# Optimization experiments

Hardware: AMD Instinct MI355X
Metric: run time of the kernel (lower is better)

The kernel has to match this reference:

```python
import jax, jax.numpy as jnp
import numpy as np

WORD_DEPTH, K, K2, L, FL, J = 128, 128, 128, 64, 3, 2


def conv1d(x, w, b):
    # x: [B, C, T], w: [O, I, k], VALID padding (matches nn.Conv1d default)
    y = jax.lax.conv_general_dilated(x, w, (1,), 'VALID',
                                     dimension_numbers=('NCH', 'OIH', 'NCH'))
    return y + b[None, :, None]


def encode(x, w1, b1, w2, b2, ws, bs):
    # x: [B, T, D] -> semantic vector [B, L]
    h = jnp.tanh(conv1d(x.transpose(0, 2, 1), w1, b1))   # [B, K, T-2]
    h = jnp.tanh(conv1d(h, w2, b2))                      # [B, K2, T-4]
    h = h.max(axis=2)                                    # kmax pooling, k=1
    return jnp.tanh(h @ ws.T + bs)                       # [B, L]


def setup_inputs() -> dict:
    key = jax.random.key(0)
    ks = jax.random.split(key, 20)
    B, T = 64, 2048
    s = 0.05
    return {
        'q':    jax.random.normal(ks[0], (B, T, WORD_DEPTH), jnp.float32),
        'pos':  jax.random.normal(ks[1], (B, T, WORD_DEPTH), jnp.float32),
        'negs': jax.random.normal(ks[2], (J, B, T, WORD_DEPTH), jnp.float32),
        'qw1': jax.random.normal(ks[3], (K, WORD_DEPTH, FL), jnp.float32) * s,
        'qb1': jnp.zeros((K,), jnp.float32),
        'qw2': jax.random.normal(ks[4], (K2, K, FL), jnp.float32) * s,
        'qb2': jnp.zeros((K2,), jnp.float32),
        'qsw': jax.random.normal(ks[5], (L, K2), jnp.float32) * s,
        'qsb': jnp.zeros((L,), jnp.float32),
        'dw1': jax.random.normal(ks[6], (K, WORD_DEPTH, FL), jnp.float32) * s,
        'db1': jnp.zeros((K,), jnp.float32),
        'dw2': jax.random.normal(ks[7], (K2, K, FL), jnp.float32) * s,
        'db2': jnp.zeros((K2,), jnp.float32),
        'dsw': jax.random.normal(ks[8], (L, K2), jnp.float32) * s,
        'dsb': jnp.zeros((L,), jnp.float32),
        'gw':  jnp.asarray(1.0, jnp.float32),   # learn_gamma Conv1d(1,1,1) weight
        'gb':  jnp.asarray(0.0, jnp.float32),   # learn_gamma bias
    }


def reference(q, pos, negs, qw1, qb1, qw2, qb2, qsw, qsb,
              dw1, db1, dw2, db2, dsw, dsb, gw, gb):
    Jn, B, T, D = negs.shape
    q_s = encode(q, qw1, qb1, qw2, qb2, qsw, qsb)                  # [B, L]
    pos_s = encode(pos, dw1, db1, dw2, db2, dsw, dsb)              # [B, L]
    neg_s = encode(negs.reshape(Jn * B, T, D),
                   dw1, db1, dw2, db2, dsw, dsb).reshape(Jn, B, L)
    pos_dot = jnp.einsum('bl,bl->b', q_s, pos_s)                   # [B]
    neg_dot = jnp.einsum('bl,jbl->bj', q_s, neg_s)                 # [B, J]
    dots = jnp.concatenate([pos_dot[:, None], neg_dot], axis=1)   # [B, J+1]
    with_gamma = gw * dots + gb                                    # conv1x1
    return jax.nn.softmax(with_gamma, axis=1)                      # [B, J+1]
```

## Files before the change

### kernel.cpp

```cpp
#include <hip/hip_runtime.h>
#include <stdint.h>


typedef __bf16 bf16x8 __attribute__((ext_vector_type(8)));
typedef __bf16 bf16x4 __attribute__((ext_vector_type(4)));
typedef float f32x16 __attribute__((ext_vector_type(16)));
typedef unsigned short u16x8 __attribute__((ext_vector_type(8)));

__device__ __forceinline__ unsigned short f2bf(float f) {
  unsigned u = __builtin_bit_cast(unsigned, f);
  u = u + 0x7FFFu + ((u >> 16) & 1u);
  return (unsigned short)(u >> 16);
}

__device__ __forceinline__ float fast_tanh(float x) {
  x = fminf(10.0f, fmaxf(-10.0f, x));
  float t = __builtin_amdgcn_exp2f(x * -2.8853900817779268f);
  return (1.0f - t) * __builtin_amdgcn_rcpf(1.0f + t);
}

__global__ void prep_kernel(const float* __restrict__ qw1, const float* __restrict__ qw2,
                            const float* __restrict__ dw1, const float* __restrict__ dw2,
                            unsigned short* __restrict__ W1f, unsigned short* __restrict__ W2f) {
  int gid = blockIdx.x * 256 + threadIdx.x;
  int which = gid >= 98304;
  int e = which ? gid - 98304 : gid;
  int br = e / 49152; int r = e % 49152;
  int f = r / 16384; int r2 = r & 16383;
  int kk = r2 >> 11; int row = (r2 >> 4) & 127; int hi = (r2 >> 3) & 1; int j = r2 & 7;
  int c = kk * 16 + hi * 8 + j;
  const float* src = which ? (br ? dw2 : qw2) : (br ? dw1 : qw1);
  (which ? W2f : W1f)[e] = f2bf(src[row * 384 + c * 3 + f]);
}

#define XS0    0
#define XBUF   16384
#define H1S0   32768
#define HBUF   15872
#define B1_OFF 64512
#define LDS_TOTAL 65024
#define YS 60
#define NWIN 35
#define TOUT 2044

__global__ __launch_bounds__(512) void cdssm_main(
    const float* __restrict__ q, const float* __restrict__ pos, const float* __restrict__ negs,
    const unsigned short* __restrict__ W1f, const unsigned short* __restrict__ W2f,
    const float* __restrict__ qb1, const float* __restrict__ db1,
    float* __restrict__ hpart) {
  extern __shared__ char lds[];
  const int tid = threadIdx.x;
  const int seq = blockIdx.x;
  const int branch = (seq < 64) ? 0 : 1;
  const float* xptr = (seq < 64) ? (q + (size_t)seq * 2048 * 128)
                    : (seq < 128) ? (pos + (size_t)(seq - 64) * 2048 * 128)
                                  : (negs + (size_t)(seq - 128) * 2048 * 128);
  const float* b1g = branch ? db1 : qb1;

  if (tid < 128) ((float*)(lds + B1_OFF))[tid] = b1g[tid];

  const int lane = tid & 63;
  const int w = tid >> 6;
  const int lrow = lane & 31;
  const int hi5 = lane >> 5;
  const int role = w >> 2;
  const int kt = w & 3;
  const int hi16 = hi5 * 16;

  const unsigned short* wfb = (role ? W2f : W1f) + (size_t)branch * 49152
                              + (kt * 32 + lrow) * 16 + hi5 * 8;

  bf16x8 ap[16];
#pragma unroll
  for (int f = 0; f < 2; ++f)
#pragma unroll
    for (int kk = 0; kk < 8; ++kk)
      ap[f * 8 + kk] = __builtin_bit_cast(bf16x8,
          *(const u16x8*)(wfb + f * 16384 + kk * 2048));

  float vmax[16];
#pragma unroll
  for (int r = 0; r < 16; ++r) vmax[r] = -1e30f;

  const int slot_s = tid >> 4;
  const int d0_s = (tid & 15) * 8;

#pragma unroll
  for (int u = 0; u < 2; ++u) {
    int sl = slot_s + u * 32;
    int t = sl;
    const float* src = xptr + ((size_t)t * 128 + d0_s);
    float4 v0 = *(const float4*)src;
    float4 v1 = *(const float4*)(src + 4);
    bf16x8 o;
    o[0] = (__bf16)v0.x; o[1] = (__bf16)v0.y; o[2] = (__bf16)v0.z; o[3] = (__bf16)v0.w;
    o[4] = (__bf16)v1.x; o[5] = (__bf16)v1.y; o[6] = (__bf16)v1.z; o[7] = (__bf16)v1.w;
    *(bf16x8*)(lds + XS0 + sl * 256 + ((d0_s * 2) ^ ((sl & 15) << 4))) = o;
  }
  __syncthreads();

  for (int i = 0; i <= NWIN; ++i) {
    float4 va[4];
    const bool doStage = (i < NWIN - 1);
    if (doStage) {
      const int tb = (i + 1) * YS;
#pragma unroll
      for (int u = 0; u < 2; ++u) {
        int t = tb + slot_s + u * 32; if (t > 2047) t = 2047;
        const float* src = xptr + ((size_t)t * 128 + d0_s);
        va[2 * u]     = *(const float4*)src;
        va[2 * u + 1] = *(const float4*)(src + 4);
      }
    }

    if (role == 0) {
      if (i < NWIN) {
        const int xb = XS0 + (i & 1) * XBUF;
        f32x16 acc0, acc1;
#pragma unroll
        for (int r = 0; r < 16; ++r) { acc0[r] = 0.f; acc1[r] = 0.f; }
        __builtin_amdgcn_s_setprio(1);
#pragma unroll
        for (int f = 0; f < 2; ++f) {
          int sv0 = lrow + f;
          int sv1 = 32 + lrow + f; if (sv1 > 63) sv1 = 63;
          int b0 = xb + sv0 * 256, z0 = (sv0 & 15) << 4;
          int b1 = xb + sv1 * 256, z1 = (sv1 & 15) << 4;
#pragma unroll
          for (int kk = 0; kk < 8; ++kk) {
            int ko = kk * 32 + hi16;
            bf16x8 bv0 = __builtin_bit_cast(bf16x8,
                *(const u16x8*)(lds + b0 + (ko ^ z0)));
            acc0 = __builtin_amdgcn_mfma_f32_32x32x16_bf16(ap[f * 8 + kk], bv0, acc0, 0, 0, 0);
            bf16x8 bv1 = __builtin_bit_cast(bf16x8,
                *(const u16x8*)(lds + b1 + (ko ^ z1)));
            acc1 = __builtin_amdgcn_mfma_f32_32x32x16_bf16(ap[f * 8 + kk], bv1, acc1, 0, 0, 0);
          }
        }
        {
          int sv0 = lrow + 2;
          int sv1 = 32 + lrow + 2; if (sv1 > 63) sv1 = 63;
          int b0 = xb + sv0 * 256, z0 = (sv0 & 15) << 4;
          int b1 = xb + sv1 * 256, z1 = (sv1 & 15) << 4;
#pragma unroll
          for (int kk = 0; kk < 8; ++kk) {
            bf16x8 av = __builtin_bit_cast(bf16x8,
                *(const u16x8*)(wfb + 2 * 16384 + kk * 2048));
            int ko = kk * 32 + hi16;
            bf16x8 bv0 = __builtin_bit_cast(bf16x8,
                *(const u16x8*)(lds + b0 + (ko ^ z0)));
            acc0 = __builtin_amdgcn_mfma_f32_32x32x16_bf16(av, bv0, acc0, 0, 0, 0);
            bf16x8 bv1 = __builtin_bit_cast(bf16x8,
                *(const u16x8*)(lds + b1 + (ko ^ z1)));
            acc1 = __builtin_amdgcn_mfma_f32_32x32x16_bf16(av, bv1, acc1, 0, 0, 0);
          }
        }
        __builtin_amdgcn_s_setprio(0);
        const int hb = H1S0 + (i & 1) * HBUF;
#pragma unroll
        for (int p = 0; p < 2; ++p) {
          const f32x16 acc = p ? acc1 : acc0;
          int s = p * 32 + lrow;
          if (s < 62) {
            int wb2 = hb + s * 256;
            int wz = (s & 15) << 4;
#pragma unroll
            for (int qd = 0; qd < 4; ++qd) {
              int k0 = kt * 32 + qd * 8 + hi5 * 4;
              float4 bq = *(const float4*)(lds + B1_OFF + k0 * 4);
              bf16x4 hv;
              hv[0] = (__bf16)fast_tanh(acc[qd * 4 + 0] + bq.x);
              hv[1] = (__bf16)fast_tanh(acc[qd * 4 + 1] + bq.y);
              hv[2] = (__bf16)fast_tanh(acc[qd * 4 + 2] + bq.z);
              hv[3] = (__bf16)fast_tanh(acc[qd * 4 + 3] + bq.w);
              *(bf16x4*)(lds + wb2 + ((k0 * 2) ^ wz)) = hv;
            }
          }
        }
      }
    } else {
      if (i >= 1) {
        const int hb = H1S0 + ((i & 1) ^ 1) * HBUF;
        f32x16 acc0, acc1;
#pragma unroll
        for (int r = 0; r < 16; ++r) { acc0[r] = 0.f; acc1[r] = 0.f; }
        __builtin_amdgcn_s_setprio(1);
#pragma unroll
        for (int f = 0; f < 2; ++f) {
          int sv0 = lrow + f;
          int sv1 = 32 + lrow + f; if (sv1 > 61) sv1 = 61;
          int b0 = hb + sv0 * 256, z0 = (sv0 & 15) << 4;
          int b1 = hb + sv1 * 256, z1 = (sv1 & 15) << 4;
#pragma unroll
          for (int kk = 0; kk < 8; ++kk) {
            int ko = kk * 32 + hi16;
            bf16x8 bv0 = __builtin_bit_cast(bf16x8,
                *(const u16x8*)(lds + b0 + (ko ^ z0)));
            acc0 = __builtin_amdgcn_mfma_f32_32x32x16_bf16(ap[f * 8 + kk], bv0, acc0, 0, 0, 0);
            bf16x8 bv1 = __builtin_bit_cast(bf16x8,
                *(const u16x8*)(lds + b1 + (ko ^ z1)));
            acc1 = __builtin_amdgcn_mfma_f32_32x32x16_bf16(ap[f * 8 + kk], bv1, acc1, 0, 0, 0);
          }
        }
        {
          int sv0 = lrow + 2;
          int sv1 = 32 + lrow + 2; if (sv1 > 61) sv1 = 61;
          int b0 = hb + sv0 * 256, z0 = (sv0 & 15) << 4;
          int b1 = hb + sv1 * 256, z1 = (sv1 & 15) << 4;
#pragma unroll
          for (int kk = 0; kk < 8; ++kk) {
            bf16x8 av = __builtin_bit_cast(bf16x8,
                *(const u16x8*)(wfb + 2 * 16384 + kk * 2048));
            int ko = kk * 32 + hi16;
            bf16x8 bv0 = __builtin_bit_cast(bf16x8,
                *(const u16x8*)(lds + b0 + (ko ^ z0)));
            acc0 = __builtin_amdgcn_mfma_f32_32x32x16_bf16(av, bv0, acc0, 0, 0, 0);
            bf16x8 bv1 = __builtin_bit_cast(bf16x8,
                *(const u16x8*)(lds + b1 + (ko ^ z1)));
            acc1 = __builtin_amdgcn_mfma_f32_32x32x16_bf16(av, bv1, acc1, 0, 0, 0);
          }
        }
        __builtin_amdgcn_s_setprio(0);
        const int base = (i - 1) * YS;
        const bool valid0 = (base + lrow < TOUT);
        const int s2b = 32 + lrow;
        const bool valid1 = (s2b < YS) && (base + s2b < TOUT);
#pragma unroll
        for (int r = 0; r < 16; ++r) {
          float v0 = valid0 ? acc0[r] : -1e30f;
          float v1 = valid1 ? acc1[r] : -1e30f;
          vmax[r] = fmaxf(vmax[r], fmaxf(v0, v1));
        }
      }
    }

    if (doStage) {
      const int xbn = XS0 + ((i + 1) & 1) * XBUF;
#pragma unroll
      for (int u = 0; u < 2; ++u) {
        int sl = slot_s + u * 32;
        const float* f0 = (const float*)&va[2 * u];
        bf16x8 o;
#pragma unroll
        for (int j = 0; j < 8; ++j) o[j] = (__bf16)f0[j];
        *(bf16x8*)(lds + xbn + sl * 256 + ((d0_s * 2) ^ ((sl & 15) << 4))) = o;
      }
    }
    __syncthreads();
  }

  if (role == 1) {
#pragma unroll
    for (int r = 0; r < 16; ++r) {
      float v = vmax[r];
      v = fmaxf(v, __shfl_xor(v, 1, 64));
      v = fmaxf(v, __shfl_xor(v, 2, 64));
      v = fmaxf(v, __shfl_xor(v, 4, 64));
      v = fmaxf(v, __shfl_xor(v, 8, 64));
      v = fmaxf(v, __shfl_xor(v, 16, 64));
      vmax[r] = v;
    }
  }
  float* hbuf = (float*)(lds + XS0);
  if (role == 1 && lrow == 0) {
#pragma unroll
    for (int r = 0; r < 16; ++r) {
      int rl = (r & 3) + 8 * (r >> 2) + 4 * hi5;
      hbuf[kt * 32 + rl] = vmax[r];
    }
  }
  __syncthreads();
  if (tid < 128) hpart[(size_t)seq * 128 + tid] = hbuf[tid];
}

__global__ void k2_proj(const float* __restrict__ hpart,
                        const float* __restrict__ qsw, const float* __restrict__ qsb,
                        const float* __restrict__ dsw, const float* __restrict__ dsb,
                        const float* __restrict__ qb2, const float* __restrict__ db2,
                        float* __restrict__ s_out) {
  int seq = blockIdx.x;
  int l = threadIdx.x;
  const float* sw = (seq < 64) ? qsw : dsw;
  const float* sb = (seq < 64) ? qsb : dsb;
  const float* b2 = (seq < 64) ? qb2 : db2;
  const float* h0 = hpart + (size_t)seq * 128;
  float acc = sb[l];
  for (int k = 0; k < 128; ++k)
    acc += fast_tanh(h0[k] + b2[k]) * sw[l * 128 + k];
  s_out[(size_t)seq * 64 + l] = fast_tanh(acc);
}

__global__ void k3_softmax(const float* __restrict__ s_out,
                           const float* __restrict__ gw, const float* __restrict__ gb,
                           float* __restrict__ out) {
  int b = threadIdx.x;
  const float* qs = s_out + (size_t)b * 64;
  const float* ps = s_out + (size_t)(64 + b) * 64;
  const float* n0 = s_out + (size_t)(128 + b) * 64;
  const float* n1 = s_out + (size_t)(192 + b) * 64;
  float d0 = 0.f, d1 = 0.f, d2 = 0.f;
  for (int l = 0; l < 64; ++l) {
    float v = qs[l];
    d0 += v * ps[l];
    d1 += v * n0[l];
    d2 += v * n1[l];
  }
  float g = gw[0], bb = gb[0];
  d0 = g * d0 + bb; d1 = g * d1 + bb; d2 = g * d2 + bb;
  float m = fmaxf(d0, fmaxf(d1, d2));
  float e0 = expf(d0 - m), e1 = expf(d1 - m), e2 = expf(d2 - m);
  float inv = 1.0f / (e0 + e1 + e2);
  out[b * 3 + 0] = e0 * inv;
  out[b * 3 + 1] = e1 * inv;
  out[b * 3 + 2] = e2 * inv;
}

extern "C" void kernel_launch(void* const* d_in, const int* in_sizes, int n_in,
                              void* d_out, int out_size, void* d_ws, size_t ws_size,
                              hipStream_t stream) {
  const float* q    = (const float*)d_in[0];
  const float* pos  = (const float*)d_in[1];
  const float* negs = (const float*)d_in[2];
  const float* qw1  = (const float*)d_in[3];
  const float* qb1  = (const float*)d_in[4];
  const float* qw2  = (const float*)d_in[5];
  const float* qb2  = (const float*)d_in[6];
  const float* qsw  = (const float*)d_in[7];
  const float* qsb  = (const float*)d_in[8];
  const float* dw1  = (const float*)d_in[9];
  const float* db1  = (const float*)d_in[10];
  const float* dw2  = (const float*)d_in[11];
  const float* db2  = (const float*)d_in[12];
  const float* dsw  = (const float*)d_in[13];
  const float* dsb  = (const float*)d_in[14];
  const float* gw   = (const float*)d_in[15];
  const float* gb   = (const float*)d_in[16];
  float* out = (float*)d_out;

  char* ws = (char*)d_ws;
  unsigned short* W1f = (unsigned short*)(ws);
  unsigned short* W2f = (unsigned short*)(ws + 196608);
  float* hpart        = (float*)(ws + 393216);
  float* s_out        = (float*)(ws + 524288);

  hipFuncSetAttribute((const void*)cdssm_main,
                      hipFuncAttributeMaxDynamicSharedMemorySize, LDS_TOTAL);

  prep_kernel<<<768, 256, 0, stream>>>(qw1, qw2, dw1, dw2, W1f, W2f);
  cdssm_main<<<256, 512, LDS_TOTAL, stream>>>(q, pos, negs, W1f, W2f, qb1, db1, hpart);
  k2_proj<<<256, 64, 0, stream>>>(hpart, qsw, qsb, dsw, dsb, qb2, db2, s_out);
  k3_softmax<<<1, 64, 0, stream>>>(s_out, gw, gb, out);
}
```

Baseline: 135.7 us.

## Double window size to 128 rows to cut barriers and halo recompute

Grows each pipeline window from 64 to 128 time steps (124 useful outputs), halving the number of windows and block-wide barriers and cutting the fraction of halo rows recomputed per window. Each window is processed as two 64-row halves inside an inner loop, and the next window's global loads are split across those halves so the staging registers stay the same size. LDS use roughly doubles to about 128 KB, which limits occupancy to one block per CU and may need the launch's dynamic shared memory size raised (LDS_TOTAL).

```diff
diff --git a/kernel.cpp b/kernel.cpp
--- a/kernel.cpp
+++ b/kernel.cpp
@@ -34,13 +34,13 @@
 }
 
 #define XS0    0
-#define XBUF   16384
-#define H1S0   32768
-#define HBUF   15872
-#define B1_OFF 64512
-#define LDS_TOTAL 65024
-#define YS 60
-#define NWIN 35
+#define XBUF   32768
+#define H1S0   65536
+#define HBUF   32256
+#define B1_OFF 130048
+#define LDS_TOTAL 130560
+#define YS 124
+#define NWIN 17
 #define TOUT 2044
 
 __global__ __launch_bounds__(512) void cdssm_main(
@@ -82,12 +82,12 @@
 #pragma unroll
   for (int r = 0; r < 16; ++r) vmax[r] = -1e30f;
 
-  const int slot_s = tid >> 4;
   const int d0_s = (tid & 15) * 8;
 
 #pragma unroll
-  for (int u = 0; u < 2; ++u) {
-    int sl = slot_s + u * 32;
+  for (int u = 0; u < 4; ++u) {
+    int c2 = tid + 512 * u;
+    int sl = c2 >> 4;
     int t = sl;
     const float* src = xptr + ((size_t)t * 128 + d0_s);
     float4 v0 = *(const float4*)src;
@@ -102,148 +102,178 @@
   for (int i = 0; i <= NWIN; ++i) {
     float4 va[4];
     const bool doStage = (i < NWIN - 1);
+    const int tb = (i + 1) * YS;
+    const int xbn = XS0 + ((i + 1) & 1) * XBUF;
+
     if (doStage) {
-      const int tb = (i + 1) * YS;
 #pragma unroll
       for (int u = 0; u < 2; ++u) {
-        int t = tb + slot_s + u * 32; if (t > 2047) t = 2047;
+        int c2 = tid + 512 * u;
+        int t = tb + (c2 >> 4); if (t > 2047) t = 2047;
         const float* src = xptr + ((size_t)t * 128 + d0_s);
         va[2 * u]     = *(const float4*)src;
         va[2 * u + 1] = *(const float4*)(src + 4);
       }
     }
 
-    if (role == 0) {
-      if (i < NWIN) {
-        const int xb = XS0 + (i & 1) * XBUF;
-        f32x16 acc0, acc1;
-#pragma unroll
-        for (int r = 0; r < 16; ++r) { acc0[r] = 0.f; acc1[r] = 0.f; }
-        __builtin_amdgcn_s_setprio(1);
-#pragma unroll
-        for (int f = 0; f < 2; ++f) {
-          int sv0 = lrow + f;
-          int sv1 = 32 + lrow + f; if (sv1 > 63) sv1 = 63;
-          int b0 = xb + sv0 * 256, z0 = (sv0 & 15) << 4;
-          int b1 = xb + sv1 * 256, z1 = (sv1 & 15) << 4;
-#pragma unroll
-          for (int kk = 0; kk < 8; ++kk) {
-            int ko = kk * 32 + hi16;
-            bf16x8 bv0 = __builtin_bit_cast(bf16x8,
-                *(const u16x8*)(lds + b0 + (ko ^ z0)));
-            acc0 = __builtin_amdgcn_mfma_f32_32x32x16_bf16(ap[f * 8 + kk], bv0, acc0, 0, 0, 0);
-            bf16x8 bv1 = __builtin_bit_cast(bf16x8,
-                *(const u16x8*)(lds + b1 + (ko ^ z1)));
-            acc1 = __builtin_amdgcn_mfma_f32_32x32x16_bf16(ap[f * 8 + kk], bv1, acc1, 0, 0, 0);
+#pragma unroll 1
+    for (int p = 0; p < 2; ++p) {
+      const int cbase = p * 64;
+
+      if (role == 0) {
+        if (i < NWIN) {
+          const int xb = XS0 + (i & 1) * XBUF;
+          f32x16 acc0, acc1;
+#pragma unroll
+          for (int r = 0; r < 16; ++r) { acc0[r] = 0.f; acc1[r] = 0.f; }
+          __builtin_amdgcn_s_setprio(1);
+#pragma unroll
+          for (int f = 0; f < 2; ++f) {
+            int sv0 = cbase + lrow + f;
+            int sv1 = cbase + 32 + lrow + f; if (sv1 > 127) sv1 = 127;
+            int b0 = xb + sv0 * 256, z0 = (sv0 & 15) << 4;
+            int b1 = xb + sv1 * 256, z1 = (sv1 & 15) << 4;
+#pragma unroll
+            for (int kk = 0; kk < 8; ++kk) {
+              int ko = kk * 32 + hi16;
+              bf16x8 bv0 = __builtin_bit_cast(bf16x8,
+                  *(const u16x8*)(lds + b0 + (ko ^ z0)));
+              acc0 = __builtin_amdgcn_mfma_f32_32x32x16_bf16(ap[f * 8 + kk], bv0, acc0, 0, 0, 0);
+              bf16x8 bv1 = __builtin_bit_cast(bf16x8,
+                  *(const u16x8*)(lds + b1 + (ko ^ z1)));
+              acc1 = __builtin_amdgcn_mfma_f32_32x32x16_bf16(ap[f * 8 + kk], bv1, acc1, 0, 0, 0);
+            }
+          }
+          {
+            int sv0 = cbase + lrow + 2;
+            int sv1 = cbase + 32 + lrow + 2; if (sv1 > 127) sv1 = 127;
+            int b0 = xb + sv0 * 256, z0 = (sv0 & 15) << 4;
+            int b1 = xb + sv1 * 256, z1 = (sv1 & 15) << 4;
+#pragma unroll
+            for (int kk = 0; kk < 8; ++kk) {
+              bf16x8 av = __builtin_bit_cast(bf16x8,
+                  *(const u16x8*)(wfb + 2 * 16384 + kk * 2048));
+              int ko = kk * 32 + hi16;
+              bf16x8 bv0 = __builtin_bit_cast(bf16x8,
+                  *(const u16x8*)(lds + b0 + (ko ^ z0)));
+              acc0 = __builtin_amdgcn_mfma_f32_32x32x16_bf16(av, bv0, acc0, 0, 0, 0);
+              bf16x8 bv1 = __builtin_bit_cast(bf16x8,
+                  *(const u16x8*)(lds + b1 + (ko ^ z1)));
+              acc1 = __builtin_amdgcn_mfma_f32_32x32x16_bf16(av, bv1, acc1, 0, 0, 0);
+            }
+          }
+          __builtin_amdgcn_s_setprio(0);
+          const int hb = H1S0 + (i & 1) * HBUF;
+#pragma unroll
+          for (int pp = 0; pp < 2; ++pp) {
+            const f32x16 acc = pp ? acc1 : acc0;
+            int s = cbase + pp * 32 + lrow;
+            if (s < 126) {
+              int wb2 = hb + s * 256;
+              int wz = (s & 15) << 4;
+#pragma unroll
+              for (int qd = 0; qd < 4; ++qd) {
+                int k0 = kt * 32 + qd * 8 + hi5 * 4;
+                float4 bq = *(const float4*)(lds + B1_OFF + k0 * 4);
+                bf16x4 hv;
+                hv[0] = (__bf16)fast_tanh(acc[qd * 4 + 0] + bq.x);
+                hv[1] = (__bf16)fast_tanh(acc[qd * 4 + 1] + bq.y);
+                hv[2] = (__bf16)fast_tanh(acc[qd * 4 + 2] + bq.z);
+                hv[3] = (__bf16)fast_tanh(acc[qd * 4 + 3] + bq.w);
+                *(bf16x4*)(lds + wb2 + ((k0 * 2) ^ wz)) = hv;
+              }
+            }
           }
         }
-        {
-          int sv0 = lrow + 2;
-          int sv1 = 32 + lrow + 2; if (sv1 > 63) sv1 = 63;
-          int b0 = xb + sv0 * 256, z0 = (sv0 & 15) << 4;
-          int b1 = xb + sv1 * 256, z1 = (sv1 & 15) << 4;
-#pragma unroll
-          for (int kk = 0; kk < 8; ++kk) {
-            bf16x8 av = __builtin_bit_cast(bf16x8,
-                *(const u16x8*)(wfb + 2 * 16384 + kk * 2048));
-            int ko = kk * 32 + hi16;
-            bf16x8 bv0 = __builtin_bit_cast(bf16x8,
-                *(const u16x8*)(lds + b0 + (ko ^ z0)));
-            acc0 = __builtin_amdgcn_mfma_f32_32x32x16_bf16(av, bv0, acc0, 0, 0, 0);
-            bf16x8 bv1 = __builtin_bit_cast(bf16x8,
-                *(const u16x8*)(lds + b1 + (ko ^ z1)));
-            acc1 = __builtin_amdgcn_mfma_f32_32x32x16_bf16(av, bv1, acc1, 0, 0, 0);
-          }
-        }
-        __builtin_amdgcn_s_setprio(0);
-        const int hb = H1S0 + (i & 1) * HBUF;
-#pragma unroll
-        for (int p = 0; p < 2; ++p) {
-          const f32x16 acc = p ? acc1 : acc0;
-          int s = p * 32 + lrow;
-          if (s < 62) {
-            int wb2 = hb + s * 256;
-            int wz = (s & 15) << 4;
-#pragma unroll
-            for (int qd = 0; qd < 4; ++qd) {
-              int k0 = kt * 32 + qd * 8 + hi5 * 4;
-              float4 bq = *(const float4*)(lds + B1_OFF + k0 * 4);
-              bf16x4 hv;
-              hv[0] = (__bf16)fast_tanh(acc[qd * 4 + 0] + bq.x);
-              hv[1] = (__bf16)fast_tanh(acc[qd * 4 + 1] + bq.y);
-              hv[2] = (__bf16)fast_tanh(acc[qd * 4 + 2] + bq.z);
-              hv[3] = (__bf16)fast_tanh(acc[qd * 4 + 3] + bq.w);
-              *(bf16x4*)(lds + wb2 + ((k0 * 2) ^ wz)) = hv;
-            }
+      } else {
+        if (i >= 1) {
+          const int hb = H1S0 + ((i & 1) ^ 1) * HBUF;
+          f32x16 acc0, acc1;
+#pragma unroll
+          for (int r = 0; r < 16; ++r) { acc0[r] = 0.f; acc1[r] = 0.f; }
+          __builtin_amdgcn_s_setprio(1);
+#pragma unroll
+          for (int f = 0; f < 2; ++f) {
+            int sv0 = cbase + lrow + f;
+            int sv1 = cbase + 32 + lrow + f; if (sv1 > 125) sv1 = 125;
+            int b0 = hb + sv0 * 256, z0 = (sv0 & 15) << 4;
+            int b1 = hb + sv1 * 256, z1 = (sv1 & 15) << 4;
+#pragma unroll
+            for (int kk = 0; kk < 8; ++kk) {
+              int ko = kk * 32 + hi16;
+              bf16x8 bv0 = __builtin_bit_cast(bf16x8,
+                  *(const u16x8*)(lds + b0 + (ko ^ z0)));
+              acc0 = __builtin_amdgcn_mfma_f32_32x32x16_bf16(ap[f * 8 + kk], bv0, acc0, 0, 0, 0);
+              bf16x8 bv1 = __builtin_bit_cast(bf16x8,
+                  *(const u16x8*)(lds + b1 + (ko ^ z1)));
+              acc1 = __builtin_amdgcn_mfma_f32_32x32x16_bf16(ap[f * 8 + kk], bv1, acc1, 0, 0, 0);
+            }
+          }
+          {
+            int sv0 = cbase + lrow + 2;
+            int sv1 = cbase + 32 + lrow + 2; if (sv1 > 125) sv1 = 125;
+            int b0 = hb + sv0 * 256, z0 = (sv0 & 15) << 4;
+            int b1 = hb + sv1 * 256, z1 = (sv1 & 15) << 4;
+#pragma unroll
+            for (int kk = 0; kk < 8; ++kk) {
+              bf16x8 av = __builtin_bit_cast(bf16x8,
+                  *(const u16x8*)(wfb + 2 * 16384 + kk * 2048));
+              int ko = kk * 32 + hi16;
+              bf16x8 bv0 = __builtin_bit_cast(bf16x8,
+                  *(const u16x8*)(lds + b0 + (ko ^ z0)));
+              acc0 = __builtin_amdgcn_mfma_f32_32x32x16_bf16(av, bv0, acc0, 0, 0, 0);
+              bf16x8 bv1 = __builtin_bit_cast(bf16x8,
+                  *(const u16x8*)(lds + b1 + (ko ^ z1)));
+              acc1 = __builtin_amdgcn_mfma_f32_32x32x16_bf16(av, bv1, acc1, 0, 0, 0);
+            }
+          }
+          __builtin_amdgcn_s_setprio(0);
+          const int base = (i - 1) * YS;
+          const int c0 = cbase + lrow;
+          const int c1 = cbase + 32 + lrow;
+          const bool valid0 = (c0 < YS) && (base + c0 < TOUT);
+          const bool valid1 = (c1 < YS) && (base + c1 < TOUT);
+#pragma unroll
+          for (int r = 0; r < 16; ++r) {
+            float v0 = valid0 ? acc0[r] : -1e30f;
+            float v1 = valid1 ? acc1[r] : -1e30f;
+            vmax[r] = fmaxf(vmax[r], fmaxf(v0, v1));
           }
         }
       }
-    } else {
-      if (i >= 1) {
-        const int hb = H1S0 + ((i & 1) ^ 1) * HBUF;
-        f32x16 acc0, acc1;
-#pragma unroll
-        for (int r = 0; r < 16; ++r) { acc0[r] = 0.f; acc1[r] = 0.f; }
-        __builtin_amdgcn_s_setprio(1);
-#pragma unroll
-        for (int f = 0; f < 2; ++f) {
-          int sv0 = lrow + f;
-          int sv1 = 32 + lrow + f; if (sv1 > 61) sv1 = 61;
-          int b0 = hb + sv0 * 256, z0 = (sv0 & 15) << 4;
-          int b1 = hb + sv1 * 256, z1 = (sv1 & 15) << 4;
-#pragma unroll
-          for (int kk = 0; kk < 8; ++kk) {
-            int ko = kk * 32 + hi16;
-            bf16x8 bv0 = __builtin_bit_cast(bf16x8,
-                *(const u16x8*)(lds + b0 + (ko ^ z0)));
-            acc0 = __builtin_amdgcn_mfma_f32_32x32x16_bf16(ap[f * 8 + kk], bv0, acc0, 0, 0, 0);
-            bf16x8 bv1 = __builtin_bit_cast(bf16x8,
-                *(const u16x8*)(lds + b1 + (ko ^ z1)));
-            acc1 = __builtin_amdgcn_mfma_f32_32x32x16_bf16(ap[f * 8 + kk], bv1, acc1, 0, 0, 0);
+
+      if (doStage) {
+        if (p == 0) {
+#pragma unroll
+          for (int u = 0; u < 2; ++u) {
+            int c2 = tid + 512 * u;
+            int sl = c2 >> 4;
+            const float* f0 = (const float*)&va[2 * u];
+            bf16x8 o;
+#pragma unroll
+            for (int j = 0; j < 8; ++j) o[j] = (__bf16)f0[j];
+            *(bf16x8*)(lds + xbn + sl * 256 + ((d0_s * 2) ^ ((sl & 15) << 4))) = o;
+          }
+#pragma unroll
+          for (int u = 0; u < 2; ++u) {
+            int c2 = tid + 512 * (u + 2);
+            int t = tb + (c2 >> 4); if (t > 2047) t = 2047;
+            const float* src = xptr + ((size_t)t * 128 + d0_s);
+            va[2 * u]     = *(const float4*)src;
+            va[2 * u + 1] = *(const float4*)(src + 4);
+          }
+        } else {
+#pragma unroll
+          for (int u = 0; u < 2; ++u) {
+            int c2 = tid + 512 * (u + 2);
+            int sl = c2 >> 4;
+            const float* f0 = (const float*)&va[2 * u];
+            bf16x8 o;
+#pragma unroll
+            for (int j = 0; j < 8; ++j) o[j] = (__bf16)f0[j];
+            *(bf16x8*)(lds + xbn + sl * 256 + ((d0_s * 2) ^ ((sl & 15) << 4))) = o;
           }
         }
-        {
-          int sv0 = lrow + 2;
-          int sv1 = 32 + lrow + 2; if (sv1 > 61) sv1 = 61;
-          int b0 = hb + sv0 * 256, z0 = (sv0 & 15) << 4;
-          int b1 = hb + sv1 * 256, z1 = (sv1 & 15) << 4;
-#pragma unroll
-          for (int kk = 0; kk < 8; ++kk) {
-            bf16x8 av = __builtin_bit_cast(bf16x8,
-                *(const u16x8*)(wfb + 2 * 16384 + kk * 2048));
-            int ko = kk * 32 + hi16;
-            bf16x8 bv0 = __builtin_bit_cast(bf16x8,
-                *(const u16x8*)(lds + b0 + (ko ^ z0)));
-            acc0 = __builtin_amdgcn_mfma_f32_32x32x16_bf16(av, bv0, acc0, 0, 0, 0);
-            bf16x8 bv1 = __builtin_bit_cast(bf16x8,
-                *(const u16x8*)(lds + b1 + (ko ^ z1)));
-            acc1 = __builtin_amdgcn_mfma_f32_32x32x16_bf16(av, bv1, acc1, 0, 0, 0);
-          }
-        }
-        __builtin_amdgcn_s_setprio(0);
-        const int base = (i - 1) * YS;
-        const bool valid0 = (base + lrow < TOUT);
-        const int s2b = 32 + lrow;
-        const bool valid1 = (s2b < YS) && (base + s2b < TOUT);
-#pragma unroll
-        for (int r = 0; r < 16; ++r) {
-          float v0 = valid0 ? acc0[r] : -1e30f;
-          float v1 = valid1 ? acc1[r] : -1e30f;
-          vmax[r] = fmaxf(vmax[r], fmaxf(v0, v1));
-        }
-      }
-    }
-
-    if (doStage) {
-      const int xbn = XS0 + ((i + 1) & 1) * XBUF;
-#pragma unroll
-      for (int u = 0; u < 2; ++u) {
-        int sl = slot_s + u * 32;
-        const float* f0 = (const float*)&va[2 * u];
-        bf16x8 o;
-#pragma unroll
-        for (int j = 0; j < 8; ++j) o[j] = (__bf16)f0[j];
-        *(bf16x8*)(lds + xbn + sl * 256 + ((d0_s * 2) ^ ((sl & 15) << 4))) = o;
       }
     }
     __syncthreads();
```

New measurement: 142.3 us. 1.05x slower.
